# Optimization experiments

Hardware: AMD Instinct MI355X
Metric: run time of the kernel (lower is better)

The kernel has to match this reference:

```python
import jax, jax.numpy as jnp
import numpy as np

THRESHOLD = 0.5
ALPHA = 1.0
N, D = 100000, 256
B, K = 1024, 128


def _l2norm(x):
    # F.normalize(x, p=2, dim=-1) with eps=1e-12
    return x / jnp.maximum(jnp.linalg.norm(x, axis=-1, keepdims=True), 1e-12)


def setup_inputs() -> dict:
    key = jax.random.key(0)
    k1, k2, k3, k4, k5, k6, k7 = jax.random.split(key, 7)
    feature = jax.random.normal(k1, (N, D), dtype=jnp.float32)
    text_embedding = jax.random.normal(k2, (N, D), dtype=jnp.float32)
    virtual = jax.random.normal(k3, (1, D), dtype=jnp.float32)
    # Gumbel(0,1) noise for gumbel_softmax (tau=1), materialized for determinism
    u = jax.random.uniform(k4, (B, K, K), dtype=jnp.float32, minval=1e-6, maxval=1.0 - 1e-6)
    gumbel = -jnp.log(-jnp.log(u))
    ego_nodes = jnp.sort(jax.random.randint(k5, (B, K), 0, N, dtype=jnp.int32), axis=-1)
    edges_adj = jax.random.randint(k6, (B, K, K), 0, 2, dtype=jnp.int32)
    train_label = jax.random.randint(k7, (B,), 0, 2, dtype=jnp.int32)
    return {"feature": feature, "text_embedding": text_embedding, "virtual": virtual,
            "gumbel": gumbel, "ego_nodes": ego_nodes, "edges_adj": edges_adj,
            "train_label": train_label}


def reference(feature, text_embedding, virtual, gumbel, ego_nodes, edges_adj, train_label):
    feat = _l2norm(feature)          # self.feature (normalized in __init__)
    emb = _l2norm(text_embedding)    # self.embedding
    te_local = _l2norm(emb - virtual)            # [N, D]

    tb = te_local[ego_nodes]                     # [B, K, D] gather per ego-subgraph
    sim = jnp.einsum('bkd,bjd->bkj', tb, tb) - THRESHOLD   # [B, K, K]
    sim_sub = jax.nn.softmax(sim + gumbel, axis=-1)         # gumbel_softmax, tau=1

    adj = edges_adj.astype(sim_sub.dtype)        # scatter edges_adj[src,dst]=1, precomputed
    # s_diff: row-wise L2 norm then mean over rows
    s_diff = jnp.sqrt(jnp.sum((adj - sim_sub) ** 2, axis=-1)).mean(axis=-1)   # [B]

    emb_out = feat[ego_nodes].mean(axis=1)       # [B, D] sum(feature)/n
    emb_pg = emb[ego_nodes].mean(axis=1)         # [B, D] sum(embedding)/n  (n == K)
    f_diff = jnp.linalg.norm(emb_out - emb_pg, axis=-1)                        # [B]

    score = s_diff + ALPHA * f_diff
    score = (score - score.min()) / (score.max() - score.min())

    y = train_label.astype(score.dtype)
    eps = 1e-7  # stabilizes log at exact 0/1 (torch BCELoss clamps log at -100)
    sc = jnp.clip(score, eps, 1.0 - eps)
    bce = -(y * jnp.log(sc) + (1.0 - y) * jnp.log1p(-sc)).mean()
    loss = bce / y.shape[0]
    return score, loss
```

## Files before the change

kernel.cpp:

```cpp
#include <hip/hip_runtime.h>
#include <hip/hip_bf16.h>
#include <math.h>

#define DIM 256
#define BB 1024
#define KK 128
#define PITCH 264

typedef __attribute__((ext_vector_type(8))) short short8;
typedef __attribute__((ext_vector_type(4))) float float4v;

__device__ __forceinline__ float dot4(const float4 a, const float4 b) {
    return a.x*b.x + a.y*b.y + a.z*b.z + a.w*b.w;
}

__device__ __forceinline__ unsigned bf2bits(float a, float b) {
    float2 t; t.x = a; t.y = b;
    __hip_bfloat162 h = __float22bfloat162_rn(t);
    unsigned u; __builtin_memcpy(&u, &h, 4);
    return u;
}

__global__ __launch_bounds__(512, 4) void fused_main(
    const float* __restrict__ feature,
    const float* __restrict__ text,
    const float* __restrict__ virt,
    const float* __restrict__ gumbel,
    const int*   __restrict__ ego,
    const int*   __restrict__ adj,
    float*       __restrict__ score_raw)
{
    __shared__ unsigned short tbs[KK * PITCH];
    __shared__ float fpart[8][DIM];
    __shared__ float spart[8];

    const int b    = blockIdx.x;
    const int tid  = threadIdx.x;
    const int wave = tid >> 6;
    const int lane = tid & 63;
    const int g    = lane >> 4;
    const int c    = lane & 15;

    float4 vm[4];
    #pragma unroll
    for (int m = 0; m < 4; ++m) vm[m] = *(const float4*)(virt + 64*m + 4*c);

    float vv2 = 0.f;
    #pragma unroll
    for (int m = 0; m < 4; ++m) vv2 += dot4(vm[m], vm[m]);
    #pragma unroll
    for (int msk = 1; msk < 16; msk <<= 1) vv2 += __shfl_xor(vv2, msk);

    const int* ego_b = ego + b * KK;
    const int  base  = wave * 16;

    int eidx[4];
    #pragma unroll
    for (int it = 0; it < 4; ++it) eidx[it] = ego_b[base + it*4 + g];

    float4 fd[4];
    #pragma unroll
    for (int m = 0; m < 4; ++m) fd[m] = make_float4(0.f, 0.f, 0.f, 0.f);

    float4 nt[4], nf[4];
    {
        const float* tr = text    + (size_t)eidx[0] * DIM + 4*c;
        const float* fr = feature + (size_t)eidx[0] * DIM + 4*c;
        #pragma unroll
        for (int m = 0; m < 4; ++m) {
            nt[m] = *(const float4*)(tr + 64*m);
            nf[m] = *(const float4*)(fr + 64*m);
        }
    }

    #pragma unroll
    for (int it = 0; it < 4; ++it) {
        float4 ct[4], cf[4];
        #pragma unroll
        for (int m = 0; m < 4; ++m) { ct[m] = nt[m]; cf[m] = nf[m]; }
        if (it < 3) {
            const float* tr = text    + (size_t)eidx[it+1] * DIM + 4*c;
            const float* fr = feature + (size_t)eidx[it+1] * DIM + 4*c;
            #pragma unroll
            for (int m = 0; m < 4; ++m) {
                nt[m] = *(const float4*)(tr + 64*m);
                nf[m] = *(const float4*)(fr + 64*m);
            }
        }

        float st = 0.f, sf = 0.f, sv = 0.f;
        #pragma unroll
        for (int m = 0; m < 4; ++m) {
            st += dot4(ct[m], ct[m]);
            sf += dot4(cf[m], cf[m]);
            sv += dot4(ct[m], vm[m]);
        }
        #pragma unroll
        for (int msk = 1; msk < 16; msk <<= 1) {
            st += __shfl_xor(st, msk);
            sf += __shfl_xor(sf, msk);
            sv += __shfl_xor(sv, msk);
        }

        const float inv_ne = __builtin_amdgcn_rsqf(fmaxf(st, 1e-24f));
        const float inv_nf = __builtin_amdgcn_rsqf(fmaxf(sf, 1e-24f));
        const float nw2    = fmaxf(1.f + vv2 - 2.f * sv * inv_ne, 1e-24f);
        const float inv_nt = __builtin_amdgcn_rsqf(nw2);

        const int row = base + it*4 + g;
        unsigned short* dst = &tbs[row * PITCH + 4*c];
        #pragma unroll
        for (int m = 0; m < 4; ++m) {
            const float e0 = ct[m].x * inv_ne, e1 = ct[m].y * inv_ne;
            const float e2 = ct[m].z * inv_ne, e3 = ct[m].w * inv_ne;
            fd[m].x += cf[m].x * inv_nf - e0;
            fd[m].y += cf[m].y * inv_nf - e1;
            fd[m].z += cf[m].z * inv_nf - e2;
            fd[m].w += cf[m].w * inv_nf - e3;
            uint2 pk;
            pk.x = bf2bits((e0 - vm[m].x) * inv_nt, (e1 - vm[m].y) * inv_nt);
            pk.y = bf2bits((e2 - vm[m].z) * inv_nt, (e3 - vm[m].w) * inv_nt);
            *(uint2*)(dst + 64*m) = pk;
        }
    }

    #pragma unroll
    for (int msk = 16; msk < 64; msk <<= 1) {
        #pragma unroll
        for (int m = 0; m < 4; ++m) {
            fd[m].x += __shfl_xor(fd[m].x, msk);
            fd[m].y += __shfl_xor(fd[m].y, msk);
            fd[m].z += __shfl_xor(fd[m].z, msk);
            fd[m].w += __shfl_xor(fd[m].w, msk);
        }
    }
    if (g == 0) {
        #pragma unroll
        for (int m = 0; m < 4; ++m)
            *(float4*)&fpart[wave][64*m + 4*c] = fd[m];
    }

    const float* gb = gumbel + (size_t)b * KK * KK;
    const int*   ab = adj    + (size_t)b * KK * KK;
    float gvv[32];
    #pragma unroll
    for (int r = 0; r < 4; ++r) {
        const float* gr = gb + (base + g*4 + r) * KK + c;
        #pragma unroll
        for (int t = 0; t < 8; ++t)
            gvv[r*8 + t] = __builtin_nontemporal_load(gr + t*16);
    }

    __syncthreads();

    float4v acc[8];
    const float4v zero = {0.f, 0.f, 0.f, 0.f};
    #pragma unroll
    for (int t = 0; t < 8; ++t) acc[t] = zero;

    #pragma unroll
    for (int q = 0; q < 8; ++q) {
        const int dq = q * 32 + g * 8;
        const short8 afr = *(const short8*)&tbs[(base + c) * PITCH + dq];
        #pragma unroll
        for (int t = 0; t < 8; ++t) {
            const short8 bfr = *(const short8*)&tbs[(t*16 + c) * PITCH + dq];
            acc[t] = __builtin_amdgcn_mfma_f32_16x16x32_bf16(afr, bfr, acc[t], 0, 0, 0);
        }
    }

    int avv[32];
    #pragma unroll
    for (int r = 0; r < 4; ++r) {
        const int* ar = ab + (base + g*4 + r) * KK + c;
        #pragma unroll
        for (int t = 0; t < 8; ++t)
            avv[r*8 + t] = __builtin_nontemporal_load(ar + t*16);
    }

    float rs = 0.f;
    #pragma unroll
    for (int r = 0; r < 4; ++r) {
        float s = 0.f, a2 = 0.f, a3 = 0.f;
        int   ia = 0;
        #pragma unroll
        for (int t = 0; t < 8; ++t) {
            const float vt = acc[t][r] - 0.5f + gvv[r*8 + t];
            const float et = __expf(vt);
            const int   ad = avv[r*8 + t];
            s  += et;
            a3 += et * et;
            ia += ad;
            a2 += ad ? et : 0.f;
        }
        #pragma unroll
        for (int msk = 1; msk < 16; msk <<= 1) {
            s  += __shfl_xor(s,  msk);
            a2 += __shfl_xor(a2, msk);
            a3 += __shfl_xor(a3, msk);
            ia += __shfl_xor(ia, msk);
        }
        const float invS = __builtin_amdgcn_rcpf(s);
        const float T = (float)ia - invS * (2.f * a2 - invS * a3);
        rs += sqrtf(fmaxf(T, 0.f));
    }
    rs += __shfl_xor(rs, 16);
    rs += __shfl_xor(rs, 32);
    if (lane == 0) spart[wave] = rs;
    __syncthreads();

    if (wave == 0) {
        float d0 = 0.f, d1 = 0.f, d2 = 0.f, d3 = 0.f;
        #pragma unroll
        for (int w = 0; w < 8; ++w) {
            d0 += fpart[w][lane];
            d1 += fpart[w][lane + 64];
            d2 += fpart[w][lane + 128];
            d3 += fpart[w][lane + 192];
        }
        const float inv = 1.f / 128.f;
        d0 *= inv; d1 *= inv; d2 *= inv; d3 *= inv;
        float q2 = d0*d0 + d1*d1 + d2*d2 + d3*d3;
        #pragma unroll
        for (int m = 1; m < 64; m <<= 1) q2 += __shfl_xor(q2, m);
        if (lane == 0) {
            float stot = 0.f;
            #pragma unroll
            for (int w = 0; w < 8; ++w) stot += spart[w];
            score_raw[b] = stot * (1.f / 128.f) + sqrtf(q2);
        }
    }
}

__global__ __launch_bounds__(1024) void finalize(
    const float* __restrict__ score_raw,
    const int*   __restrict__ label,
    float*       __restrict__ out)
{
    __shared__ float wmin[16], wmax[16], wsum[16];
    const int tid = threadIdx.x;
    const float s = score_raw[tid];
    float mn = s, mx = s;
    #pragma unroll
    for (int m = 1; m < 64; m <<= 1) {
        mn = fminf(mn, __shfl_xor(mn, m));
        mx = fmaxf(mx, __shfl_xor(mx, m));
    }
    if ((tid & 63) == 0) { wmin[tid >> 6] = mn; wmax[tid >> 6] = mx; }
    __syncthreads();
    float gmn = wmin[0], gmx = wmax[0];
    #pragma unroll
    for (int w = 1; w < 16; ++w) {
        gmn = fminf(gmn, wmin[w]);
        gmx = fmaxf(gmx, wmax[w]);
    }
    const float score = (s - gmn) / (gmx - gmn);
    out[tid] = score;

    const float y  = (float)label[tid];
    const float sc = fminf(fmaxf(score, 1e-7f), 1.f - 1e-7f);
    float term = -(y * logf(sc) + (1.f - y) * log1pf(-sc));
    #pragma unroll
    for (int m = 1; m < 64; m <<= 1) term += __shfl_xor(term, m);
    if ((tid & 63) == 0) wsum[tid >> 6] = term;
    __syncthreads();
    if (tid == 0) {
        float tot = 0.f;
        #pragma unroll
        for (int w = 0; w < 16; ++w) tot += wsum[w];
        out[BB] = tot / (1024.f * 1024.f);
    }
}

extern "C" void kernel_launch(void* const* d_in, const int* in_sizes, int n_in,
                              void* d_out, int out_size, void* d_ws, size_t ws_size,
                              hipStream_t stream) {
    const float* feature = (const float*)d_in[0];
    const float* text    = (const float*)d_in[1];
    const float* virt    = (const float*)d_in[2];
    const float* gumbel  = (const float*)d_in[3];
    const int*   ego     = (const int*)d_in[4];
    const int*   adj     = (const int*)d_in[5];
    const int*   label   = (const int*)d_in[6];
    float* out       = (float*)d_out;
    float* score_raw = (float*)d_ws;

    fused_main<<<BB, 512, 0, stream>>>(feature, text, virt, gumbel, ego, adj, score_raw);
    finalize<<<1, 1024, 0, stream>>>(score_raw, label, out);
}
```

Before: 81.06 us.

## Deepen gather prefetch, issue adjacency loads before MFMA, pack adjacency to bitmask

Row gathers of text and feature now run two deep instead of one, so each wave keeps more global loads in flight. The adjacency loads are issued before the gumbel loads and the MFMA loop, and are packed into a 32-bit mask partway through the matrix multiply. That hides their latency behind compute and frees the 32 integer registers they occupied. Launch bounds are written as explicit AMDGPU attributes. The deeper prefetch raises register pressure, which could cause spills at the 4-waves-per-EU target.

After: 90.90 us. 1.12x slower.

```diff
diff --git a/kernel.cpp b/kernel.cpp
--- a/kernel.cpp
+++ b/kernel.cpp
@@ -21,7 +21,9 @@
     return u;
 }
 
-__global__ __launch_bounds__(512, 4) void fused_main(
+__global__ __attribute__((amdgpu_flat_work_group_size(512, 512),
+                          amdgpu_waves_per_eu(4, 4)))
+void fused_main(
     const float* __restrict__ feature,
     const float* __restrict__ text,
     const float* __restrict__ virt,
@@ -62,29 +64,31 @@
     #pragma unroll
     for (int m = 0; m < 4; ++m) fd[m] = make_float4(0.f, 0.f, 0.f, 0.f);
 
-    float4 nt[4], nf[4];
-    {
-        const float* tr = text    + (size_t)eidx[0] * DIM + 4*c;
-        const float* fr = feature + (size_t)eidx[0] * DIM + 4*c;
+    float4 snt[2][4], snf[2][4];
+    #pragma unroll
+    for (int p = 0; p < 2; ++p) {
+        const float* tr = text    + (size_t)eidx[p] * DIM + 4*c;
+        const float* fr = feature + (size_t)eidx[p] * DIM + 4*c;
         #pragma unroll
         for (int m = 0; m < 4; ++m) {
-            nt[m] = *(const float4*)(tr + 64*m);
-            nf[m] = *(const float4*)(fr + 64*m);
+            snt[p][m] = *(const float4*)(tr + 64*m);
+            snf[p][m] = *(const float4*)(fr + 64*m);
         }
     }
 
     #pragma unroll
     for (int it = 0; it < 4; ++it) {
+        const int sl = it & 1;
         float4 ct[4], cf[4];
         #pragma unroll
-        for (int m = 0; m < 4; ++m) { ct[m] = nt[m]; cf[m] = nf[m]; }
-        if (it < 3) {
-            const float* tr = text    + (size_t)eidx[it+1] * DIM + 4*c;
-            const float* fr = feature + (size_t)eidx[it+1] * DIM + 4*c;
+        for (int m = 0; m < 4; ++m) { ct[m] = snt[sl][m]; cf[m] = snf[sl][m]; }
+        if (it < 2) {
+            const float* tr = text    + (size_t)eidx[it+2] * DIM + 4*c;
+            const float* fr = feature + (size_t)eidx[it+2] * DIM + 4*c;
             #pragma unroll
             for (int m = 0; m < 4; ++m) {
-                nt[m] = *(const float4*)(tr + 64*m);
-                nf[m] = *(const float4*)(fr + 64*m);
+                snt[sl][m] = *(const float4*)(tr + 64*m);
+                snf[sl][m] = *(const float4*)(fr + 64*m);
             }
         }
 
@@ -142,6 +146,14 @@
 
     const float* gb = gumbel + (size_t)b * KK * KK;
     const int*   ab = adj    + (size_t)b * KK * KK;
+    int atmp[32];
+    #pragma unroll
+    for (int r = 0; r < 4; ++r) {
+        const int* ar = ab + (base + g*4 + r) * KK + c;
+        #pragma unroll
+        for (int t = 0; t < 8; ++t)
+            atmp[r*8 + t] = __builtin_nontemporal_load(ar + t*16);
+    }
     float gvv[32];
     #pragma unroll
     for (int r = 0; r < 4; ++r) {
@@ -159,7 +171,7 @@
     for (int t = 0; t < 8; ++t) acc[t] = zero;
 
     #pragma unroll
-    for (int q = 0; q < 8; ++q) {
+    for (int q = 0; q < 2; ++q) {
         const int dq = q * 32 + g * 8;
         const short8 afr = *(const short8*)&tbs[(base + c) * PITCH + dq];
         #pragma unroll
@@ -168,40 +180,43 @@
             acc[t] = __builtin_amdgcn_mfma_f32_16x16x32_bf16(afr, bfr, acc[t], 0, 0, 0);
         }
     }
-
-    int avv[32];
+    unsigned am = 0;
+    #pragma unroll
+    for (int i = 0; i < 32; ++i) am |= (atmp[i] ? 1u : 0u) << i;
+    #pragma unroll
+    for (int q = 2; q < 8; ++q) {
+        const int dq = q * 32 + g * 8;
+        const short8 afr = *(const short8*)&tbs[(base + c) * PITCH + dq];
+        #pragma unroll
+        for (int t = 0; t < 8; ++t) {
+            const short8 bfr = *(const short8*)&tbs[(t*16 + c) * PITCH + dq];
+            acc[t] = __builtin_amdgcn_mfma_f32_16x16x32_bf16(afr, bfr, acc[t], 0, 0, 0);
+        }
+    }
+
+    float rs = 0.f;
     #pragma unroll
     for (int r = 0; r < 4; ++r) {
-        const int* ar = ab + (base + g*4 + r) * KK + c;
-        #pragma unroll
-        for (int t = 0; t < 8; ++t)
-            avv[r*8 + t] = __builtin_nontemporal_load(ar + t*16);
-    }
-
-    float rs = 0.f;
-    #pragma unroll
-    for (int r = 0; r < 4; ++r) {
+        const unsigned mr = (am >> (r*8)) & 0xffu;
         float s = 0.f, a2 = 0.f, a3 = 0.f;
-        int   ia = 0;
         #pragma unroll
         for (int t = 0; t < 8; ++t) {
             const float vt = acc[t][r] - 0.5f + gvv[r*8 + t];
             const float et = __expf(vt);
-            const int   ad = avv[r*8 + t];
             s  += et;
             a3 += et * et;
-            ia += ad;
-            a2 += ad ? et : 0.f;
-        }
+            a2 += ((mr >> t) & 1u) ? et : 0.f;
+        }
+        float fia = (float)__popc(mr);
         #pragma unroll
         for (int msk = 1; msk < 16; msk <<= 1) {
-            s  += __shfl_xor(s,  msk);
-            a2 += __shfl_xor(a2, msk);
-            a3 += __shfl_xor(a3, msk);
-            ia += __shfl_xor(ia, msk);
+            s   += __shfl_xor(s,   msk);
+            a2  += __shfl_xor(a2,  msk);
+            a3  += __shfl_xor(a3,  msk);
+            fia += __shfl_xor(fia, msk);
         }
         const float invS = __builtin_amdgcn_rcpf(s);
-        const float T = (float)ia - invS * (2.f * a2 - invS * a3);
+        const float T = fia - invS * (2.f * a2 - invS * a3);
         rs += sqrtf(fmaxf(T, 0.f));
     }
     rs += __shfl_xor(rs, 16);
```

## Double block threads, one wave per row in gather, split MFMA columns across wave pairs

Applied to the files above, without the earlier changes.

The fused kernel now runs 1024 threads per block instead of 512. In the gather phase each wave handles one row at a time with a full-wave float4 load and a two-deep prefetch. In the MFMA phase each 16-row strip is split between two waves, each taking half the columns. Per-row softmax partial sums go through shared memory and are combined in an extra reduction stage, and the adjacency values are packed into a bitmask to save registers. The aim is more memory parallelism and fewer registers per thread, at the cost of extra barriers and 64-lane shuffle reductions for every row.

Result: faster. 76.03 us (-6.2%).

```diff
diff --git a/kernel.cpp b/kernel.cpp
--- a/kernel.cpp
+++ b/kernel.cpp
@@ -21,7 +21,7 @@
     return u;
 }
 
-__global__ __launch_bounds__(512, 4) void fused_main(
+__global__ __launch_bounds__(1024, 8) void fused_main(
     const float* __restrict__ feature,
     const float* __restrict__ text,
     const float* __restrict__ virt,
@@ -31,75 +31,51 @@
     float*       __restrict__ score_raw)
 {
     __shared__ unsigned short tbs[KK * PITCH];
-    __shared__ float fpart[8][DIM];
-    __shared__ float spart[8];
+    __shared__ float fpart8[8][DIM];
+    __shared__ float rowpart[KK][8];
+    __shared__ float spart[2];
 
     const int b    = blockIdx.x;
     const int tid  = threadIdx.x;
     const int wave = tid >> 6;
     const int lane = tid & 63;
-    const int g    = lane >> 4;
-    const int c    = lane & 15;
-
-    float4 vm[4];
-    #pragma unroll
-    for (int m = 0; m < 4; ++m) vm[m] = *(const float4*)(virt + 64*m + 4*c);
-
-    float vv2 = 0.f;
-    #pragma unroll
-    for (int m = 0; m < 4; ++m) vv2 += dot4(vm[m], vm[m]);
-    #pragma unroll
-    for (int msk = 1; msk < 16; msk <<= 1) vv2 += __shfl_xor(vv2, msk);
 
     const int* ego_b = ego + b * KK;
-    const int  base  = wave * 16;
-
-    int eidx[4];
-    #pragma unroll
-    for (int it = 0; it < 4; ++it) eidx[it] = ego_b[base + it*4 + g];
-
-    float4 fd[4];
-    #pragma unroll
-    for (int m = 0; m < 4; ++m) fd[m] = make_float4(0.f, 0.f, 0.f, 0.f);
-
-    float4 nt[4], nf[4];
-    {
-        const float* tr = text    + (size_t)eidx[0] * DIM + 4*c;
-        const float* fr = feature + (size_t)eidx[0] * DIM + 4*c;
-        #pragma unroll
-        for (int m = 0; m < 4; ++m) {
-            nt[m] = *(const float4*)(tr + 64*m);
-            nf[m] = *(const float4*)(fr + 64*m);
-        }
-    }
-
-    #pragma unroll
-    for (int it = 0; it < 4; ++it) {
-        float4 ct[4], cf[4];
-        #pragma unroll
-        for (int m = 0; m < 4; ++m) { ct[m] = nt[m]; cf[m] = nf[m]; }
-        if (it < 3) {
-            const float* tr = text    + (size_t)eidx[it+1] * DIM + 4*c;
-            const float* fr = feature + (size_t)eidx[it+1] * DIM + 4*c;
-            #pragma unroll
-            for (int m = 0; m < 4; ++m) {
-                nt[m] = *(const float4*)(tr + 64*m);
-                nf[m] = *(const float4*)(fr + 64*m);
-            }
-        }
-
-        float st = 0.f, sf = 0.f, sv = 0.f;
-        #pragma unroll
-        for (int m = 0; m < 4; ++m) {
-            st += dot4(ct[m], ct[m]);
-            sf += dot4(cf[m], cf[m]);
-            sv += dot4(ct[m], vm[m]);
-        }
-        #pragma unroll
-        for (int msk = 1; msk < 16; msk <<= 1) {
-            st += __shfl_xor(st, msk);
-            sf += __shfl_xor(sf, msk);
-            sv += __shfl_xor(sv, msk);
+
+    const float4 vm = ((const float4*)virt)[lane];
+    float vv2 = dot4(vm, vm);
+    #pragma unroll
+    for (int m = 1; m < 64; m <<= 1) vv2 += __shfl_xor(vv2, m);
+
+    const int baseA = wave * 8;
+    int eidx[8];
+    #pragma unroll
+    for (int k = 0; k < 8; ++k) eidx[k] = ego_b[baseA + k];
+
+    float4 fdv = make_float4(0.f, 0.f, 0.f, 0.f);
+
+    float4 pt[2], pf[2];
+    #pragma unroll
+    for (int p = 0; p < 2; ++p) {
+        pt[p] = ((const float4*)(text    + (size_t)eidx[p] * DIM))[lane];
+        pf[p] = ((const float4*)(feature + (size_t)eidx[p] * DIM))[lane];
+    }
+
+    #pragma unroll
+    for (int k = 0; k < 8; ++k) {
+        const int sl = k & 1;
+        const float4 ct = pt[sl], cf = pf[sl];
+        if (k < 6) {
+            pt[sl] = ((const float4*)(text    + (size_t)eidx[k+2] * DIM))[lane];
+            pf[sl] = ((const float4*)(feature + (size_t)eidx[k+2] * DIM))[lane];
+        }
+
+        float st = dot4(ct, ct), sf = dot4(cf, cf), sv = dot4(ct, vm);
+        #pragma unroll
+        for (int m = 1; m < 64; m <<= 1) {
+            st += __shfl_xor(st, m);
+            sf += __shfl_xor(sf, m);
+            sv += __shfl_xor(sv, m);
         }
 
         const float inv_ne = __builtin_amdgcn_rsqf(fmaxf(st, 1e-24f));
@@ -107,128 +83,129 @@
         const float nw2    = fmaxf(1.f + vv2 - 2.f * sv * inv_ne, 1e-24f);
         const float inv_nt = __builtin_amdgcn_rsqf(nw2);
 
-        const int row = base + it*4 + g;
-        unsigned short* dst = &tbs[row * PITCH + 4*c];
-        #pragma unroll
-        for (int m = 0; m < 4; ++m) {
-            const float e0 = ct[m].x * inv_ne, e1 = ct[m].y * inv_ne;
-            const float e2 = ct[m].z * inv_ne, e3 = ct[m].w * inv_ne;
-            fd[m].x += cf[m].x * inv_nf - e0;
-            fd[m].y += cf[m].y * inv_nf - e1;
-            fd[m].z += cf[m].z * inv_nf - e2;
-            fd[m].w += cf[m].w * inv_nf - e3;
-            uint2 pk;
-            pk.x = bf2bits((e0 - vm[m].x) * inv_nt, (e1 - vm[m].y) * inv_nt);
-            pk.y = bf2bits((e2 - vm[m].z) * inv_nt, (e3 - vm[m].w) * inv_nt);
-            *(uint2*)(dst + 64*m) = pk;
-        }
-    }
-
-    #pragma unroll
-    for (int msk = 16; msk < 64; msk <<= 1) {
-        #pragma unroll
-        for (int m = 0; m < 4; ++m) {
-            fd[m].x += __shfl_xor(fd[m].x, msk);
-            fd[m].y += __shfl_xor(fd[m].y, msk);
-            fd[m].z += __shfl_xor(fd[m].z, msk);
-            fd[m].w += __shfl_xor(fd[m].w, msk);
-        }
-    }
-    if (g == 0) {
-        #pragma unroll
-        for (int m = 0; m < 4; ++m)
-            *(float4*)&fpart[wave][64*m + 4*c] = fd[m];
-    }
+        const float e0 = ct.x * inv_ne, e1 = ct.y * inv_ne;
+        const float e2 = ct.z * inv_ne, e3 = ct.w * inv_ne;
+        fdv.x += cf.x * inv_nf - e0;
+        fdv.y += cf.y * inv_nf - e1;
+        fdv.z += cf.z * inv_nf - e2;
+        fdv.w += cf.w * inv_nf - e3;
+
+        uint2 pk;
+        pk.x = bf2bits((e0 - vm.x) * inv_nt, (e1 - vm.y) * inv_nt);
+        pk.y = bf2bits((e2 - vm.z) * inv_nt, (e3 - vm.w) * inv_nt);
+        *(uint2*)&tbs[(baseA + k) * PITCH + 4 * lane] = pk;
+    }
+
+    if (wave & 1) *(float4*)&fpart8[wave >> 1][4 * lane] = fdv;
+
+    __syncthreads();
+
+    if (!(wave & 1)) {
+        float4 o = *(float4*)&fpart8[wave >> 1][4 * lane];
+        o.x += fdv.x; o.y += fdv.y; o.z += fdv.z; o.w += fdv.w;
+        *(float4*)&fpart8[wave >> 1][4 * lane] = o;
+    }
+
+    const int strip = wave >> 1;
+    const int half  = wave & 1;
+    const int g     = lane >> 4;
+    const int c     = lane & 15;
+    const int baseR = strip * 16;
 
     const float* gb = gumbel + (size_t)b * KK * KK;
-    const int*   ab = adj    + (size_t)b * KK * KK;
-    float gvv[32];
+    float gvv[16];
     #pragma unroll
     for (int r = 0; r < 4; ++r) {
-        const float* gr = gb + (base + g*4 + r) * KK + c;
-        #pragma unroll
-        for (int t = 0; t < 8; ++t)
-            gvv[r*8 + t] = __builtin_nontemporal_load(gr + t*16);
-    }
-
-    __syncthreads();
-
-    float4v acc[8];
+        const float* gr = gb + (baseR + g*4 + r) * KK + half*64 + c;
+        #pragma unroll
+        for (int t = 0; t < 4; ++t)
+            gvv[r*4 + t] = __builtin_nontemporal_load(gr + t*16);
+    }
+
+    float4v acc[4];
     const float4v zero = {0.f, 0.f, 0.f, 0.f};
     #pragma unroll
-    for (int t = 0; t < 8; ++t) acc[t] = zero;
+    for (int t = 0; t < 4; ++t) acc[t] = zero;
 
     #pragma unroll
     for (int q = 0; q < 8; ++q) {
         const int dq = q * 32 + g * 8;
-        const short8 afr = *(const short8*)&tbs[(base + c) * PITCH + dq];
-        #pragma unroll
-        for (int t = 0; t < 8; ++t) {
-            const short8 bfr = *(const short8*)&tbs[(t*16 + c) * PITCH + dq];
+        const short8 afr = *(const short8*)&tbs[(baseR + c) * PITCH + dq];
+        #pragma unroll
+        for (int t = 0; t < 4; ++t) {
+            const short8 bfr = *(const short8*)&tbs[(half*64 + t*16 + c) * PITCH + dq];
             acc[t] = __builtin_amdgcn_mfma_f32_16x16x32_bf16(afr, bfr, acc[t], 0, 0, 0);
         }
     }
 
-    int avv[32];
+    const int* ab = adj + (size_t)b * KK * KK;
+    unsigned am = 0;
     #pragma unroll
     for (int r = 0; r < 4; ++r) {
-        const int* ar = ab + (base + g*4 + r) * KK + c;
-        #pragma unroll
-        for (int t = 0; t < 8; ++t)
-            avv[r*8 + t] = __builtin_nontemporal_load(ar + t*16);
-    }
-
-    float rs = 0.f;
+        const int* ar = ab + (baseR + g*4 + r) * KK + half*64 + c;
+        #pragma unroll
+        for (int t = 0; t < 4; ++t)
+            am |= (__builtin_nontemporal_load(ar + t*16) ? 1u : 0u) << (r*4 + t);
+    }
+
     #pragma unroll
     for (int r = 0; r < 4; ++r) {
+        const unsigned mr = (am >> (r*4)) & 0xFu;
         float s = 0.f, a2 = 0.f, a3 = 0.f;
-        int   ia = 0;
-        #pragma unroll
-        for (int t = 0; t < 8; ++t) {
-            const float vt = acc[t][r] - 0.5f + gvv[r*8 + t];
+        #pragma unroll
+        for (int t = 0; t < 4; ++t) {
+            const float vt = acc[t][r] - 0.5f + gvv[r*4 + t];
             const float et = __expf(vt);
-            const int   ad = avv[r*8 + t];
             s  += et;
             a3 += et * et;
-            ia += ad;
-            a2 += ad ? et : 0.f;
-        }
+            a2 += ((mr >> t) & 1u) ? et : 0.f;
+        }
+        float fia = (float)__popc(mr);
         #pragma unroll
         for (int msk = 1; msk < 16; msk <<= 1) {
-            s  += __shfl_xor(s,  msk);
-            a2 += __shfl_xor(a2, msk);
-            a3 += __shfl_xor(a3, msk);
-            ia += __shfl_xor(ia, msk);
-        }
+            s   += __shfl_xor(s,   msk);
+            a2  += __shfl_xor(a2,  msk);
+            a3  += __shfl_xor(a3,  msk);
+            fia += __shfl_xor(fia, msk);
+        }
+        if (c == 0) {
+            float4 pk4; pk4.x = s; pk4.y = a2; pk4.z = a3; pk4.w = fia;
+            *(float4*)&rowpart[baseR + g*4 + r][half * 4] = pk4;
+        }
+    }
+
+    __syncthreads();
+
+    if (tid < KK) {
+        const float4 pa = *(const float4*)&rowpart[tid][0];
+        const float4 pb = *(const float4*)&rowpart[tid][4];
+        const float s   = pa.x + pb.x;
+        const float a2  = pa.y + pb.y;
+        const float a3  = pa.z + pb.z;
+        const float fia = pa.w + pb.w;
         const float invS = __builtin_amdgcn_rcpf(s);
-        const float T = (float)ia - invS * (2.f * a2 - invS * a3);
-        rs += sqrtf(fmaxf(T, 0.f));
-    }
-    rs += __shfl_xor(rs, 16);
-    rs += __shfl_xor(rs, 32);
-    if (lane == 0) spart[wave] = rs;
+        float sq = sqrtf(fmaxf(fia - invS * (2.f * a2 - invS * a3), 0.f));
+        #pragma unroll
+        for (int m = 1; m < 64; m <<= 1) sq += __shfl_xor(sq, m);
+        if (lane == 0) spart[wave] = sq;
+    }
+
     __syncthreads();
 
     if (wave == 0) {
-        float d0 = 0.f, d1 = 0.f, d2 = 0.f, d3 = 0.f;
-        #pragma unroll
-        for (int w = 0; w < 8; ++w) {
-            d0 += fpart[w][lane];
-            d1 += fpart[w][lane + 64];
-            d2 += fpart[w][lane + 128];
-            d3 += fpart[w][lane + 192];
+        float4 d = make_float4(0.f, 0.f, 0.f, 0.f);
+        #pragma unroll
+        for (int j = 0; j < 8; ++j) {
+            const float4 p = *(const float4*)&fpart8[j][4 * lane];
+            d.x += p.x; d.y += p.y; d.z += p.z; d.w += p.w;
         }
         const float inv = 1.f / 128.f;
-        d0 *= inv; d1 *= inv; d2 *= inv; d3 *= inv;
-        float q2 = d0*d0 + d1*d1 + d2*d2 + d3*d3;
+        d.x *= inv; d.y *= inv; d.z *= inv; d.w *= inv;
+        float q2 = dot4(d, d);
         #pragma unroll
         for (int m = 1; m < 64; m <<= 1) q2 += __shfl_xor(q2, m);
-        if (lane == 0) {
-            float stot = 0.f;
-            #pragma unroll
-            for (int w = 0; w < 8; ++w) stot += spart[w];
-            score_raw[b] = stot * (1.f / 128.f) + sqrtf(q2);
-        }
+        if (lane == 0)
+            score_raw[b] = (spart[0] + spart[1]) * (1.f / 128.f) + sqrtf(q2);
     }
 }
 
@@ -285,6 +262,6 @@
     float* out       = (float*)d_out;
     float* score_raw = (float*)d_ws;
 
-    fused_main<<<BB, 512, 0, stream>>>(feature, text, virt, gumbel, ego, adj, score_raw);
+    fused_main<<<BB, 1024, 0, stream>>>(feature, text, virt, gumbel, ego, adj, score_raw);
     finalize<<<1, 1024, 0, stream>>>(score_raw, label, out);
 }
```
